# Kernel tuning notes

Hardware: AMD Instinct MI355X
Metric: run time of the kernel (lower is better)

## Reference

```python
import jax, jax.numpy as jnp
import numpy as np

TEMPERATURE = 1.0
WEIGHT = 1.0


def _transitivity_sum(rel):
    """rel: [N, N] relation probabilities for one (batch, relation) slice.
    Computes sum_{a,b,c} relu(rel[a,b] - rel[a,c] * rel[b,c]) via a scan over c
    (outer product of column c), keeping memory at O(N^2) instead of O(N^3)."""
    def step(acc, col):  # col = rel[:, c], shape [N]
        viol = jax.nn.relu(rel - col[:, None] * col[None, :])  # [N, N]
        return acc + jnp.sum(viol), None
    acc, _ = jax.lax.scan(step, jnp.zeros((), rel.dtype), rel.T)
    return acc


def setup_inputs() -> dict:
    key = jax.random.key(0)
    B, N, R = 2, 512, 4
    relation_logits = jax.random.normal(key, (B, N, N, R), dtype=jnp.float32)
    entity_masks = jnp.ones((B, N), dtype=jnp.int32)
    return {"relation_logits": relation_logits, "entity_masks": entity_masks}


def reference(relation_logits, entity_masks):
    B, N, _, R = relation_logits.shape
    probs = jax.nn.sigmoid(relation_logits / TEMPERATURE)  # [B, N, N, R]
    m = (entity_masks > 0).astype(probs.dtype)             # [B, N]
    rel = probs * m[:, :, None, None] * m[:, None, :, None]
    # flatten (batch, relation) and vmap the per-matrix cubic reduction
    rel_br = jnp.transpose(rel, (0, 3, 1, 2)).reshape(B * R, N, N)
    per = jax.vmap(_transitivity_sum)(rel_br)              # [B*R]
    # per-batch loss = sum_r / R; final = weight * mean over batch
    return WEIGHT * jnp.sum(per) / (R * B)
```

## Files before the change

### kernel.cpp

```cpp
#include <hip/hip_runtime.h>
#include <math.h>

#define N      512
#define RNUM   4
#define BNUM   2
#define NSLICE (RNUM * BNUM)
#define TILE   128
#define CT     32
#define LSTR   136
#define CSPLIT 16
#define NCOLB  16
#define SCALE  0.0625f

typedef _Float16 half2_t __attribute__((ext_vector_type(2)));

__device__ __forceinline__ unsigned int h2u(half2_t h) {
  return __builtin_bit_cast(unsigned int, h);
}
__device__ __forceinline__ half2_t u2h(unsigned int u) {
  return __builtin_bit_cast(half2_t, u);
}

#if __has_builtin(__builtin_amdgcn_fdot2)
__device__ __forceinline__ float fdot2_(half2_t a, half2_t b, float c) {
  return __builtin_amdgcn_fdot2(a, b, c, false);
}
#else
__device__ __forceinline__ float fdot2_(half2_t a, half2_t b, float c) {
  return c + (float)a.x * (float)b.x + (float)a.y * (float)b.y;
}
#endif

__device__ __forceinline__ float sigmoidf_(float x) {
  return 1.0f / (1.0f + __expf(-x));
}

__global__ void zero_out_kernel(float* out) { out[0] = 0.0f; }

__global__ __launch_bounds__(256) void prep_f16_kernel(const float* __restrict__ logits,
                                                       const int* __restrict__ masks,
                                                       _Float16* __restrict__ P,
                                                       float* __restrict__ out) {
  if (blockIdx.x == 0 && threadIdx.x == 0) out[0] = 0.0f;
  int t = blockIdx.x * 256 + threadIdx.x;
  int b = t >> 18;
  int rem = t & (N * N - 1);
  int i = rem >> 9;
  int j = rem & (N - 1);
  float4 lg = *(const float4*)(logits + (size_t)t * 4);
  float mm = ((masks[b * N + i] > 0) && (masks[b * N + j] > 0)) ? 1.0f : 0.0f;
  size_t base = (size_t)b * RNUM * N * N + rem;
  P[base + 0 * (size_t)N * N] = (_Float16)(mm * sigmoidf_(lg.x));
  P[base + 1 * (size_t)N * N] = (_Float16)(mm * sigmoidf_(lg.y));
  P[base + 2 * (size_t)N * N] = (_Float16)(mm * sigmoidf_(lg.z));
  P[base + 3 * (size_t)N * N] = (_Float16)(mm * sigmoidf_(lg.w));
}

__global__ __launch_bounds__(256, 8) void work_f16_kernel(const _Float16* __restrict__ P,
                                                          float* __restrict__ out) {
  __shared__ __align__(16) _Float16 tA[CT][LSTR];
  __shared__ __align__(16) _Float16 tB[CT][LSTR];
  __shared__ float wsum[4];

  const int tid = threadIdx.x;
  const int bid = blockIdx.x;

  if (bid < NCOLB) {
    const int s    = bid >> 1;
    const int half = bid & 1;
    const int c    = half * 256 + tid;
    const _Float16* col = P + (size_t)s * N * N + c;
    float sum = 0.0f;
#pragma unroll 16
    for (int a = 0; a < N; ++a) sum += (float)col[(size_t)a * N];
    float v = sum * ((float)N - sum);
    for (int off = 32; off > 0; off >>= 1) v += __shfl_down(v, off, 64);
    const int wid = tid >> 6;
    if ((tid & 63) == 0) wsum[wid] = v;
    __syncthreads();
    if (tid == 0)
      atomicAdd(out, (wsum[0] + wsum[1] + wsum[2] + wsum[3]) * SCALE);
    return;
  }

  const int m  = bid - NCOLB;
  const int bt = m & 3;
  const int at = (m >> 2) & 3;
  const int s  = (m >> 4) & 7;
  const int cz = m >> 7;
  const int a0 = at * TILE;
  const int b0 = bt * TILE;
  const int c0 = cz * CT;

  const int ta = tid & 15;
  const int tb = tid >> 4;

  const _Float16* Ph = P + (size_t)s * N * N;

  {
    const int u   = tid & 127;
    const int h   = tid >> 7;
    const int isB = u >> 6;
    const int p   = u & 63;
    const int r0  = (isB ? b0 : a0) + 2 * p;
    const int cc0 = c0 + h * 16;
    const _Float16* s0row = Ph + (size_t)r0 * N + cc0;
    const _Float16* s1row = s0row + N;
    _Float16* dst = isB ? &tB[h * 16][2 * p] : &tA[h * 16][2 * p];
    uint4 q0 = ((const uint4*)s0row)[0];
    uint4 q1 = ((const uint4*)s0row)[1];
    uint4 r0v = ((const uint4*)s1row)[0];
    uint4 r1v = ((const uint4*)s1row)[1];
    unsigned int w0[8] = {q0.x, q0.y, q0.z, q0.w, q1.x, q1.y, q1.z, q1.w};
    unsigned int w1[8] = {r0v.x, r0v.y, r0v.z, r0v.w, r1v.x, r1v.y, r1v.z, r1v.w};
#pragma unroll
    for (int k = 0; k < 8; ++k) {
      unsigned int lo = (w1[k] << 16) | (w0[k] & 0xFFFFu);
      unsigned int hi = (w1[k] & 0xFFFF0000u) | (w0[k] >> 16);
      *(unsigned int*)(dst + (size_t)(2 * k) * LSTR)     = lo;
      *(unsigned int*)(dst + (size_t)(2 * k + 1) * LSTR) = hi;
    }
  }

  half2_t rab2[8][4];
#pragma unroll
  for (int x = 0; x < 8; ++x) {
    int ga = a0 + ta * 8 + x;
    uint4 q = *(const uint4*)(Ph + (size_t)ga * N + b0 + tb * 8);
    rab2[x][0] = u2h(q.x); rab2[x][1] = u2h(q.y);
    rab2[x][2] = u2h(q.z); rab2[x][3] = u2h(q.w);
  }

  float acc[8];
#pragma unroll
  for (int x = 0; x < 8; ++x) acc[x] = 0.0f;

  const half2_t kOne = {(_Float16)1.0f, (_Float16)1.0f};

  __syncthreads();

#pragma unroll 4
  for (int c = 0; c < CT; ++c) {
    uint4 ua = *(const uint4*)&tA[c][ta * 8];
    uint4 ub = *(const uint4*)&tB[c][tb * 8];
    half2_t av[4] = {u2h(ua.x), u2h(ua.y), u2h(ua.z), u2h(ua.w)};
    half2_t bv[4] = {u2h(ub.x), u2h(ub.y), u2h(ub.z), u2h(ub.w)};
#pragma unroll
    for (int x = 0; x < 8; ++x) {
      _Float16 as = (x & 1) ? av[x >> 1].y : av[x >> 1].x;
      half2_t asp = {as, as};
      float a_ = acc[x];
#pragma unroll
      for (int yp = 0; yp < 4; ++yp) {
        half2_t t2 = rab2[x][yp] - asp * bv[yp];
        half2_t p2 = u2h(h2u(t2) & 0x7FFF7FFFu);
        a_ = fdot2_(p2, kOne, a_);
      }
      acc[x] = a_;
    }
  }

  float tsum = 0.0f;
#pragma unroll
  for (int x = 0; x < 8; ++x) tsum += acc[x];

  for (int off = 32; off > 0; off >>= 1) tsum += __shfl_down(tsum, off, 64);

  const int wid = tid >> 6;
  if ((tid & 63) == 0) wsum[wid] = tsum;
  __syncthreads();
  if (tid == 0)
    atomicAdd(out, (wsum[0] + wsum[1] + wsum[2] + wsum[3]) * SCALE);
}

#define FCT    64
#define FSTR   132
#define FCSPL  4

__global__ __launch_bounds__(256, 2) void work_f32_fallback(const float* __restrict__ logits,
                                                            const int* __restrict__ masks,
                                                            float* __restrict__ out) {
  __shared__ __align__(16) float tA[FCT][FSTR];
  __shared__ __align__(16) float tB[FCT][FSTR];
  __shared__ float wsum[4];

  const int tid = threadIdx.x;
  const int bid = blockIdx.x;

  if (bid < NCOLB) {
    const int s    = bid >> 1;
    const int half = bid & 1;
    const int c    = half * 256 + tid;
    const int bb   = s >> 2;
    const int r    = s & 3;
    const int* mrow = masks + bb * N;
    float mc = (mrow[c] > 0) ? 1.0f : 0.0f;
    float sum = 0.0f;
#pragma unroll 4
    for (int a = 0; a < N; ++a) {
      float ma = (mrow[a] > 0) ? 1.0f : 0.0f;
      size_t idx = ((size_t)(bb * N + a) * N + c) * RNUM + r;
      sum += sigmoidf_(logits[idx]) * ma * mc;
    }
    float v = sum * ((float)N - sum);
    for (int off = 32; off > 0; off >>= 1) v += __shfl_down(v, off, 64);
    const int wid = tid >> 6;
    if ((tid & 63) == 0) wsum[wid] = v;
    __syncthreads();
    if (tid == 0)
      atomicAdd(out, (wsum[0] + wsum[1] + wsum[2] + wsum[3]) * SCALE);
    return;
  }

  const int m  = bid - NCOLB;
  const int bt = m & 3;
  const int at = (m >> 2) & 3;
  const int s  = (m >> 4) & 7;
  const int cz = m >> 7;
  const int a0 = at * TILE;
  const int b0 = bt * TILE;
  const int bb = s >> 2;
  const int r  = s & 3;
  const int cbeg = cz * (N / FCSPL);
  const int cend = cbeg + (N / FCSPL);

  const int ta = tid & 15;
  const int tb = tid >> 4;
  const int* mrow = masks + bb * N;

  float rab[8][8];
#pragma unroll
  for (int x = 0; x < 8; ++x) {
    int ra = a0 + ((x >> 2) << 6) + ta * 4 + (x & 3);
    float ma = (mrow[ra] > 0) ? 1.0f : 0.0f;
#pragma unroll
    for (int y = 0; y < 8; ++y) {
      int cb = b0 + ((y >> 2) << 6) + tb * 4 + (y & 3);
      float mb = (mrow[cb] > 0) ? 1.0f : 0.0f;
      size_t idx = ((size_t)(bb * N + ra) * N + cb) * RNUM + r;
      rab[x][y] = sigmoidf_(logits[idx]) * ma * mb;
    }
  }

  float acc[8][2];
#pragma unroll
  for (int x = 0; x < 8; ++x) { acc[x][0] = 0.0f; acc[x][1] = 0.0f; }

  for (int c0 = cbeg; c0 < cend; c0 += FCT) {
    __syncthreads();
#pragma unroll
    for (int it = 0; it < 32; ++it) {
      int e = it * 256 + tid;
      int c = e & 63;
      int i = e >> 6;
      int pc = ((((i >> 2) ^ ((c >> 2) & 31)) & 31) << 2) | (i & 3);
      float mc = (mrow[c0 + c] > 0) ? 1.0f : 0.0f;
      {
        float mi = (mrow[a0 + i] > 0) ? 1.0f : 0.0f;
        size_t idx = ((size_t)(bb * N + a0 + i) * N + (c0 + c)) * RNUM + r;
        tA[c][pc] = sigmoidf_(logits[idx]) * mi * mc;
      }
      {
        float mi = (mrow[b0 + i] > 0) ? 1.0f : 0.0f;
        size_t idx = ((size_t)(bb * N + b0 + i) * N + (c0 + c)) * RNUM + r;
        tB[c][pc] = sigmoidf_(logits[idx]) * mi * mc;
      }
    }
    __syncthreads();

#pragma unroll 2
    for (int cg = 0; cg < FCT / 4; ++cg) {
      const float* pa = &tA[cg * 4][((ta ^ cg) & 31) << 2];
      const float* pb = &tB[cg * 4][((tb ^ cg) & 31) << 2];
#pragma unroll
      for (int dc = 0; dc < 4; ++dc) {
        float4 a0v = *(const float4*)(pa + dc * FSTR);
        float4 a1v = *(const float4*)(pa + dc * FSTR + 64);
        float4 b0v = *(const float4*)(pb + dc * FSTR);
        float4 b1v = *(const float4*)(pb + dc * FSTR + 64);
        float avv[8] = {a0v.x, a0v.y, a0v.z, a0v.w, a1v.x, a1v.y, a1v.z, a1v.w};
        float bvv[8] = {b0v.x, b0v.y, b0v.z, b0v.w, b1v.x, b1v.y, b1v.z, b1v.w};
#pragma unroll
        for (int x = 0; x < 8; ++x) {
#pragma unroll
          for (int y = 0; y < 4; ++y)
            acc[x][0] += fabsf(fmaf(-avv[x], bvv[y], rab[x][y]));
#pragma unroll
          for (int y = 4; y < 8; ++y)
            acc[x][1] += fabsf(fmaf(-avv[x], bvv[y], rab[x][y]));
        }
      }
    }
  }

  float tsum = 0.0f;
#pragma unroll
  for (int x = 0; x < 8; ++x) tsum += acc[x][0] + acc[x][1];
  for (int off = 32; off > 0; off >>= 1) tsum += __shfl_down(tsum, off, 64);
  const int wid = tid >> 6;
  if ((tid & 63) == 0) wsum[wid] = tsum;
  __syncthreads();
  if (tid == 0)
    atomicAdd(out, (wsum[0] + wsum[1] + wsum[2] + wsum[3]) * SCALE);
}

extern "C" void kernel_launch(void* const* d_in, const int* in_sizes, int n_in,
                              void* d_out, int out_size, void* d_ws, size_t ws_size,
                              hipStream_t stream) {
  const float* logits = (const float*)d_in[0];
  const int*   masks  = (const int*)d_in[1];
  float*       out    = (float*)d_out;

  const size_t P_BYTES = (size_t)NSLICE * N * N * sizeof(_Float16);

  if (ws_size >= P_BYTES) {
    _Float16* P = (_Float16*)d_ws;
    prep_f16_kernel<<<(BNUM * N * N) / 256, 256, 0, stream>>>(logits, masks, P, out);
    const int nblocks = NCOLB + 4 * 4 * NSLICE * CSPLIT;
    work_f16_kernel<<<nblocks, 256, 0, stream>>>(P, out);
  } else {
    zero_out_kernel<<<1, 1, 0, stream>>>(out);
    const int nblocks = NCOLB + 4 * 4 * NSLICE * FCSPL;
    work_f32_fallback<<<nblocks, 256, 0, stream>>>(logits, masks, out);
  }
}
```

Measured before the change: 114.3 us.

## Use packed f16 FMA with fp16 partial accumulation and vectorize prep stores

```diff
diff --git a/kernel.cpp b/kernel.cpp
--- a/kernel.cpp
+++ b/kernel.cpp
@@ -31,8 +31,26 @@
 }
 #endif
 
+__device__ __forceinline__ unsigned pk_fnma_bl(unsigned a, unsigned b, unsigned c) {
+  unsigned d;
+  asm("v_pk_fma_f16 %0, %1, %2, %3 op_sel:[0,0,0] op_sel_hi:[0,1,1] neg_lo:[1,0,0] neg_hi:[1,0,0]"
+      : "=v"(d) : "v"(a), "v"(b), "v"(c));
+  return d;
+}
+__device__ __forceinline__ unsigned pk_fnma_bh(unsigned a, unsigned b, unsigned c) {
+  unsigned d;
+  asm("v_pk_fma_f16 %0, %1, %2, %3 op_sel:[1,0,0] op_sel_hi:[1,1,1] neg_lo:[1,0,0] neg_hi:[1,0,0]"
+      : "=v"(d) : "v"(a), "v"(b), "v"(c));
+  return d;
+}
+
 __device__ __forceinline__ float sigmoidf_(float x) {
   return 1.0f / (1.0f + __expf(-x));
+}
+
+__device__ __forceinline__ unsigned packh2(float a, float b) {
+  half2_t h = {(_Float16)a, (_Float16)b};
+  return h2u(h);
 }
 
 __global__ void zero_out_kernel(float* out) { out[0] = 0.0f; }
@@ -43,20 +61,43 @@
                                                        float* __restrict__ out) {
   if (blockIdx.x == 0 && threadIdx.x == 0) out[0] = 0.0f;
   int t = blockIdx.x * 256 + threadIdx.x;
-  int b = t >> 18;
-  int rem = t & (N * N - 1);
-  int i = rem >> 9;
-  int j = rem & (N - 1);
-  float4 lg = *(const float4*)(logits + (size_t)t * 4);
-  float mm = ((masks[b * N + i] > 0) && (masks[b * N + j] > 0)) ? 1.0f : 0.0f;
-  size_t base = (size_t)b * RNUM * N * N + rem;
-  P[base + 0 * (size_t)N * N] = (_Float16)(mm * sigmoidf_(lg.x));
-  P[base + 1 * (size_t)N * N] = (_Float16)(mm * sigmoidf_(lg.y));
-  P[base + 2 * (size_t)N * N] = (_Float16)(mm * sigmoidf_(lg.z));
-  P[base + 3 * (size_t)N * N] = (_Float16)(mm * sigmoidf_(lg.w));
-}
-
-__global__ __launch_bounds__(256, 8) void work_f16_kernel(const _Float16* __restrict__ P,
+  int b = t >> 16;
+  int rem4 = t & (N * N / 4 - 1);
+  int i = rem4 >> 7;
+  int j4 = rem4 & 127;
+  const float4* Lp = ((const float4*)logits) + ((size_t)(b * N + i) * N + 4 * j4);
+  float4 l0 = Lp[0], l1 = Lp[1], l2 = Lp[2], l3 = Lp[3];
+  int4 mj = *(const int4*)(masks + b * N + 4 * j4);
+  float mi = (masks[b * N + i] > 0) ? 1.0f : 0.0f;
+  float m0 = mi * ((mj.x > 0) ? 1.0f : 0.0f);
+  float m1 = mi * ((mj.y > 0) ? 1.0f : 0.0f);
+  float m2 = mi * ((mj.z > 0) ? 1.0f : 0.0f);
+  float m3 = mi * ((mj.w > 0) ? 1.0f : 0.0f);
+  size_t off = (size_t)i * N + 4 * j4;
+  _Float16* Pb = P + (size_t)b * RNUM * N * N + off;
+  {
+    uint2 v = {packh2(m0 * sigmoidf_(l0.x), m1 * sigmoidf_(l1.x)),
+               packh2(m2 * sigmoidf_(l2.x), m3 * sigmoidf_(l3.x))};
+    *(uint2*)(Pb + 0 * (size_t)N * N) = v;
+  }
+  {
+    uint2 v = {packh2(m0 * sigmoidf_(l0.y), m1 * sigmoidf_(l1.y)),
+               packh2(m2 * sigmoidf_(l2.y), m3 * sigmoidf_(l3.y))};
+    *(uint2*)(Pb + 1 * (size_t)N * N) = v;
+  }
+  {
+    uint2 v = {packh2(m0 * sigmoidf_(l0.z), m1 * sigmoidf_(l1.z)),
+               packh2(m2 * sigmoidf_(l2.z), m3 * sigmoidf_(l3.z))};
+    *(uint2*)(Pb + 2 * (size_t)N * N) = v;
+  }
+  {
+    uint2 v = {packh2(m0 * sigmoidf_(l0.w), m1 * sigmoidf_(l1.w)),
+               packh2(m2 * sigmoidf_(l2.w), m3 * sigmoidf_(l3.w))};
+    *(uint2*)(Pb + 3 * (size_t)N * N) = v;
+  }
+}
+
+__global__ __launch_bounds__(256, 4) void work_f16_kernel(const _Float16* __restrict__ P,
                                                           float* __restrict__ out) {
   __shared__ __align__(16) _Float16 tA[CT][LSTR];
   __shared__ __align__(16) _Float16 tB[CT][LSTR];
@@ -122,41 +163,47 @@
     }
   }
 
-  half2_t rab2[8][4];
+  unsigned rabw[8][4];
 #pragma unroll
   for (int x = 0; x < 8; ++x) {
     int ga = a0 + ta * 8 + x;
     uint4 q = *(const uint4*)(Ph + (size_t)ga * N + b0 + tb * 8);
-    rab2[x][0] = u2h(q.x); rab2[x][1] = u2h(q.y);
-    rab2[x][2] = u2h(q.z); rab2[x][3] = u2h(q.w);
+    rabw[x][0] = q.x; rabw[x][1] = q.y; rabw[x][2] = q.z; rabw[x][3] = q.w;
   }
 
   float acc[8];
-#pragma unroll
-  for (int x = 0; x < 8; ++x) acc[x] = 0.0f;
+  unsigned q16[8];
+#pragma unroll
+  for (int x = 0; x < 8; ++x) { acc[x] = 0.0f; q16[x] = 0u; }
 
   const half2_t kOne = {(_Float16)1.0f, (_Float16)1.0f};
 
   __syncthreads();
 
-#pragma unroll 4
-  for (int c = 0; c < CT; ++c) {
-    uint4 ua = *(const uint4*)&tA[c][ta * 8];
-    uint4 ub = *(const uint4*)&tB[c][tb * 8];
-    half2_t av[4] = {u2h(ua.x), u2h(ua.y), u2h(ua.z), u2h(ua.w)};
-    half2_t bv[4] = {u2h(ub.x), u2h(ub.y), u2h(ub.z), u2h(ub.w)};
+#pragma unroll 1
+  for (int cg = 0; cg < CT / 4; ++cg) {
+#pragma unroll
+    for (int dc = 0; dc < 4; ++dc) {
+      const int c = cg * 4 + dc;
+      uint4 ua = *(const uint4*)&tA[c][ta * 8];
+      uint4 ub = *(const uint4*)&tB[c][tb * 8];
+      unsigned aw[4] = {ua.x, ua.y, ua.z, ua.w};
+      unsigned bw[4] = {ub.x, ub.y, ub.z, ub.w};
+#pragma unroll
+      for (int k = 0; k < 4; ++k) {
+#pragma unroll
+        for (int yp = 0; yp < 4; ++yp) {
+          unsigned tl = pk_fnma_bl(aw[k], bw[yp], rabw[2 * k][yp]);
+          q16[2 * k] = h2u(u2h(q16[2 * k]) + u2h(tl & 0x7FFF7FFFu));
+          unsigned th = pk_fnma_bh(aw[k], bw[yp], rabw[2 * k + 1][yp]);
+          q16[2 * k + 1] = h2u(u2h(q16[2 * k + 1]) + u2h(th & 0x7FFF7FFFu));
+        }
+      }
+    }
 #pragma unroll
     for (int x = 0; x < 8; ++x) {
-      _Float16 as = (x & 1) ? av[x >> 1].y : av[x >> 1].x;
-      half2_t asp = {as, as};
-      float a_ = acc[x];
-#pragma unroll
-      for (int yp = 0; yp < 4; ++yp) {
-        half2_t t2 = rab2[x][yp] - asp * bv[yp];
-        half2_t p2 = u2h(h2u(t2) & 0x7FFF7FFFu);
-        a_ = fdot2_(p2, kOne, a_);
-      }
-      acc[x] = a_;
+      acc[x] = fdot2_(u2h(q16[x]), kOne, acc[x]);
+      q16[x] = 0u;
     }
   }
 
@@ -315,7 +362,7 @@
 
   if (ws_size >= P_BYTES) {
     _Float16* P = (_Float16*)d_ws;
-    prep_f16_kernel<<<(BNUM * N * N) / 256, 256, 0, stream>>>(logits, masks, P, out);
+    prep_f16_kernel<<<(BNUM * N * N / 4) / 256, 256, 0, stream>>>(logits, masks, P, out);
     const int nblocks = NCOLB + 4 * 4 * NSLICE * CSPLIT;
     work_f16_kernel<<<nblocks, 256, 0, stream>>>(P, out);
   } else {
```

New measurement: 115.2 us. About the same (+0.8%).
